# Performance work log

Measured on AMD Instinct MI355X. Metric: run time of the kernel, lower is better.

Reference implementation:

```python
import jax, jax.numpy as jnp
import numpy as np

L, B, D = 512, 16, 256
H = 4            # MAX_DIFF == num_heads
MAX_BONDS = 6
MAX_DIFF = 4
PROB_SHIFT = 0.3


def _attn_weights(x, Wqk, Wq, bq, Wk, bk, mask):
    """Per-head softmax(QK^T/sqrt(hd)) with key padding mask.
    x: [b,l,d]; Wqk: [d,2d] (the inc/dec_qk pre-projection);
    Wq/Wk: [d,d] (MHA in_proj, stored x@W layout); mask: [b,l] bool (True=masked).
    Returns [b,h,l,l]. The V path / out_proj of the torch MHA are discarded
    by the original module, so they are omitted here.
    """
    b, l, d = x.shape
    hd = d // H
    q = x @ Wqk[:, :d]
    k = x @ Wqk[:, d:]
    Q = (q @ Wq + bq).reshape(b, l, H, hd)
    K = (k @ Wk + bk).reshape(b, l, H, hd)
    scores = jnp.einsum('blhd,bmhd->bhlm', Q, K) / np.sqrt(hd)
    scores = jnp.where(mask[:, None, None, :], -jnp.inf, scores)
    return jax.nn.softmax(scores, axis=-1)


def setup_inputs() -> dict:
    key = jax.random.key(0)
    ks = jax.random.split(key, 16)
    s = 0.05
    p = lambda k, shape: jax.random.normal(k, shape, jnp.float32) * s
    # key_padding_mask: last 64 positions padded (True == masked)
    src_mask = jnp.broadcast_to(jnp.arange(L)[None, :] >= (L - 64), (B, L))
    return {
        'molecule_embedding': jax.random.normal(ks[0], (L, B, D), jnp.float32),
        'src_bond': jax.random.randint(ks[1], (B, L, MAX_BONDS), 0, L, jnp.int32),
        'src_mask': src_mask,
        'W_inc_qk': p(ks[2], (D, 2 * D)),
        'Wq_inc': p(ks[3], (D, D)), 'bq_inc': p(ks[4], (D,)),
        'Wk_inc': p(ks[5], (D, D)), 'bk_inc': p(ks[6], (D,)),
        'W_dec_qk': p(ks[7], (D, 2 * D)),
        'Wq_dec': p(ks[8], (D, D)), 'bq_dec': p(ks[9], (D,)),
        'Wk_dec': p(ks[10], (D, D)), 'bk_dec': p(ks[11], (D,)),
        'Wc': p(ks[12], (MAX_DIFF, MAX_DIFF)), 'bc': p(ks[13], (MAX_DIFF,)),
    }


def reference(molecule_embedding, src_bond, src_mask,
              W_inc_qk, Wq_inc, bq_inc, Wk_inc, bk_inc,
              W_dec_qk, Wq_dec, bq_dec, Wk_dec, bk_dec,
              Wc, bc):
    x = jnp.transpose(molecule_embedding, (1, 0, 2))  # [b,l,d]
    b, l, _ = x.shape

    inc = _attn_weights(x, W_inc_qk, Wq_inc, bq_inc, Wk_inc, bk_inc, src_mask)
    dec = _attn_weights(x, W_dec_qk, Wq_dec, bq_dec, Wk_dec, bk_dec, src_mask)

    pad = (~src_mask).astype(jnp.float32)              # 1 - mask
    pm2 = pad[:, :, None] * pad[:, None, :]            # [b,l,l]

    # cls_layer((inc-dec).permute(0,2,3,1)) * (MAX_DIFF*pad_mask)[...,None]
    diff = (jnp.einsum('bhlm,hc->blmc', inc - dec, Wc) + bc)
    diff = diff * (MAX_DIFF * pm2)[..., None]          # [b,l,l,4]

    # src_bond has last dim == MAX_BONDS -> one-hot neighbor counts
    src_w = jax.nn.one_hot(src_bond, l, dtype=jnp.float32).sum(axis=2) * pm2  # [b,l,l]
    eye = jnp.eye(l, dtype=jnp.float32)
    src_w = src_w * (1.0 - eye)[None]                  # zero diagonal

    # _shift_probs(src_weight.long(), prob_shift, MAX_DIFF)
    oh = jax.nn.one_hot(src_w.astype(jnp.int32), MAX_DIFF, dtype=jnp.float32)
    probs = oh * (1.0 - PROB_SHIFT) + (1.0 - oh) * (PROB_SHIFT / (MAX_DIFF - 1))
    probs = probs / probs.sum(axis=-1, keepdims=True)

    return jnp.log(probs + 1e-6) + diff                # [b,l,l,4]
```

## Files before the change

kernel.cpp:

```cpp
#include <hip/hip_runtime.h>
#include <stdint.h>

typedef unsigned short u16t;
typedef short s8v __attribute__((ext_vector_type(8)));
typedef float f4v __attribute__((ext_vector_type(4)));

#define MFMA16 __builtin_amdgcn_mfma_f32_16x16x32_bf16

#define QKN (16*4*512*64)

__device__ __forceinline__ u16t f2bf(float f) {
  unsigned u = __builtin_bit_cast(unsigned, f);
  u += 0x7fffu + ((u >> 16) & 1u);
  return (u16t)(u >> 16);
}

__global__ __launch_bounds__(256) void mask_norm(const int* __restrict__ raw,
                                                 int* __restrict__ dst) {
  __shared__ int mode;
  const int t = threadIdx.x;
  if (t == 0) mode = 0;
  __syncthreads();
  unsigned v0 = (unsigned)raw[t], v1 = (unsigned)raw[t + 256];
  if (v0 == 0x3F800000u || v1 == 0x3F800000u) mode = 2;
  __syncthreads();
  if (mode == 0 && (v0 > 1u || v1 > 1u)) mode = 1;
  __syncthreads();
  const int i = blockIdx.x * 256 + t;
  int m;
  if (mode == 2)      m = (((const float*)raw)[i] != 0.0f) ? 1 : 0;
  else if (mode == 1) m = ((const unsigned char*)raw)[i];
  else                m = raw[i];
  dst[i] = m;
}

__global__ __launch_bounds__(256) void weff_kernel(
    const float* __restrict__ Wiqk, const float* __restrict__ Wqi, const float* __restrict__ Wki,
    const float* __restrict__ Wdqk, const float* __restrict__ Wqd, const float* __restrict__ Wkd,
    u16t* __restrict__ weffT) {
  __shared__ float At[16][65];
  __shared__ float Bt[16][65];
  const int tid = threadIdx.x;
  const int n0 = blockIdx.x * 64;
  const int d0 = blockIdx.y * 64;
  const int p  = blockIdx.z;
  const float* A2  = (p == 0) ? Wqi : (p == 1) ? Wki : (p == 2) ? Wqd : Wkd;
  const float* Wqk = (p < 2) ? Wiqk : Wdqk;
  const int aoff = (p & 1) * 256;
  const int tx = tid & 15, ty = tid >> 4;

  float acc[4][4];
#pragma unroll
  for (int i = 0; i < 4; ++i)
#pragma unroll
    for (int j = 0; j < 4; ++j) acc[i][j] = 0.f;

  for (int k0 = 0; k0 < 256; k0 += 16) {
    __syncthreads();
    {
      int nn = tid & 63, kr = tid >> 6;
#pragma unroll
      for (int pass = 0; pass < 4; ++pass) {
        int kk = kr + pass * 4;
        At[kk][nn] = A2[(size_t)(k0 + kk) * 256 + n0 + nn];
      }
      int kk = tid & 15, dr = tid >> 4;
#pragma unroll
      for (int pass = 0; pass < 4; ++pass) {
        int dd = dr + pass * 16;
        Bt[kk][dd] = Wqk[(size_t)(d0 + dd) * 512 + aoff + k0 + kk];
      }
    }
    __syncthreads();
#pragma unroll
    for (int kk = 0; kk < 16; ++kk) {
      float a[4], b[4];
#pragma unroll
      for (int i = 0; i < 4; ++i) a[i] = At[kk][ty * 4 + i];
#pragma unroll
      for (int j = 0; j < 4; ++j) b[j] = Bt[kk][tx * 4 + j];
#pragma unroll
      for (int i = 0; i < 4; ++i)
#pragma unroll
        for (int j = 0; j < 4; ++j) acc[i][j] = fmaf(a[i], b[j], acc[i][j]);
    }
  }

#pragma unroll
  for (int i = 0; i < 4; ++i) {
    u16t h[4] = {f2bf(acc[i][0]), f2bf(acc[i][1]), f2bf(acc[i][2]), f2bf(acc[i][3])};
    *(uint2*)(&weffT[((size_t)(p * 256 + n0 + ty * 4 + i)) * 256 + d0 + tx * 4]) =
        *(const uint2*)h;
  }
}

__global__ __launch_bounds__(256) void proj_kernel(
    const float* __restrict__ emb, const u16t* __restrict__ weffT,
    const float* __restrict__ bq_inc, const float* __restrict__ bk_inc,
    const float* __restrict__ bq_dec, const float* __restrict__ bk_dec,
    u16t* __restrict__ qk) {
  __shared__ __align__(16) u16t As[128 * 40];
  __shared__ __align__(16) u16t Bs[128 * 40];
  const int t = threadIdx.x;
  const int n0 = blockIdx.x * 128;
  const int r0 = blockIdx.y * 128;
  const int bb = r0 >> 9;
  const int l0 = r0 & 511;
  const int lane = t & 63, wid = t >> 6;
  const int quad = lane >> 4, c15 = lane & 15;
  const int wm = wid >> 1, wn = wid & 1;

  f4v acc[4][4];
#pragma unroll
  for (int i = 0; i < 4; ++i)
#pragma unroll
    for (int j = 0; j < 4; ++j) acc[i][j] = f4v{0.f, 0.f, 0.f, 0.f};

  for (int k0 = 0; k0 < 256; k0 += 32) {
    __syncthreads();
#pragma unroll
    for (int i = 0; i < 2; ++i) {
      int c = t + i * 256;
      int m = c >> 2, off = (c & 3) * 8;
      const float* src = emb + (size_t)((l0 + m) * 16 + bb) * 256 + k0 + off;
      float4 x0 = *(const float4*)src;
      float4 x1 = *(const float4*)(src + 4);
      u16t h[8] = {f2bf(x0.x), f2bf(x0.y), f2bf(x0.z), f2bf(x0.w),
                   f2bf(x1.x), f2bf(x1.y), f2bf(x1.z), f2bf(x1.w)};
      *(uint4*)(&As[m * 40 + off]) = *(const uint4*)h;
      *(uint4*)(&Bs[m * 40 + off]) =
          *(const uint4*)(weffT + (size_t)(n0 + m) * 256 + k0 + off);
    }
    __syncthreads();
    s8v af[4], bf[4];
#pragma unroll
    for (int mi = 0; mi < 4; ++mi)
      af[mi] = *(const s8v*)(&As[(wm * 64 + mi * 16 + c15) * 40 + quad * 8]);
#pragma unroll
    for (int ni = 0; ni < 4; ++ni)
      bf[ni] = *(const s8v*)(&Bs[(wn * 64 + ni * 16 + c15) * 40 + quad * 8]);
#pragma unroll
    for (int mi = 0; mi < 4; ++mi)
#pragma unroll
      for (int ni = 0; ni < 4; ++ni)
        acc[mi][ni] = MFMA16(af[mi], bf[ni], acc[mi][ni], 0, 0, 0);
  }

  const float* biasP[4] = {bq_inc, bk_inc, bq_dec, bk_dec};
#pragma unroll
  for (int ni = 0; ni < 4; ++ni) {
    int n = n0 + wn * 64 + ni * 16 + c15;
    int p = n >> 8, h = (n >> 6) & 3, tt = n & 63, jj = n & 255;
    float bias = biasP[p][jj];
    u16t* dst = qk + (size_t)p * QKN;
#pragma unroll
    for (int mi = 0; mi < 4; ++mi) {
#pragma unroll
      for (int reg = 0; reg < 4; ++reg) {
        int l = l0 + wm * 64 + mi * 16 + quad * 4 + reg;
        dst[((size_t)(bb * 4 + h) * 512 + l) * 64 + tt] = f2bf(acc[mi][ni][reg] + bias);
      }
    }
  }
}

__global__ __launch_bounds__(256) void stats_kernel(
    const u16t* __restrict__ qk, const int* __restrict__ mask, float* __restrict__ invsum) {
  __shared__ __align__(16) u16t Qs[64 * 72];
  __shared__ __align__(16) u16t Ks[128 * 72];
  __shared__ int mrow[512];
  const int t = threadIdx.x;
  const int l0 = blockIdx.x * 64;
  const int cy = blockIdx.y;
  const int pp = cy >> 6, bb = (cy >> 2) & 15, h = cy & 3;
  const u16t* Q = qk + (size_t)(2 * pp) * QKN;
  const u16t* K = qk + (size_t)(2 * pp + 1) * QKN;
  mrow[t] = mask[bb * 512 + t];
  mrow[t + 256] = mask[bb * 512 + t + 256];
#pragma unroll
  for (int i = 0; i < 2; ++i) {
    int c = t + i * 256;
    int row = c >> 3, off = (c & 7) * 8;
    *(uint4*)(&Qs[row * 72 + off]) =
        *(const uint4*)(Q + ((size_t)(bb * 4 + h) * 512 + l0 + row) * 64 + off);
  }
  const int lane = t & 63, wid = t >> 6;
  const int quad = lane >> 4, c15 = lane & 15;
  float rs[4] = {0.f, 0.f, 0.f, 0.f};
  for (int m0 = 0; m0 < 512; m0 += 128) {
    __syncthreads();
#pragma unroll
    for (int i = 0; i < 4; ++i) {
      int c = t + i * 256;
      int row = c >> 3, off = (c & 7) * 8;
      *(uint4*)(&Ks[row * 72 + off]) =
          *(const uint4*)(K + ((size_t)(bb * 4 + h) * 512 + m0 + row) * 64 + off);
    }
    __syncthreads();
    s8v a0 = *(const s8v*)(&Qs[(wid * 16 + c15) * 72 + quad * 8]);
    s8v a1 = *(const s8v*)(&Qs[(wid * 16 + c15) * 72 + 32 + quad * 8]);
#pragma unroll
    for (int nt = 0; nt < 8; ++nt) {
      s8v b0 = *(const s8v*)(&Ks[(nt * 16 + c15) * 72 + quad * 8]);
      s8v b1 = *(const s8v*)(&Ks[(nt * 16 + c15) * 72 + 32 + quad * 8]);
      f4v sacc = f4v{0.f, 0.f, 0.f, 0.f};
      sacc = MFMA16(a0, b0, sacc, 0, 0, 0);
      sacc = MFMA16(a1, b1, sacc, 0, 0, 0);
      int m = m0 + nt * 16 + c15;
      if (!mrow[m]) {
#pragma unroll
        for (int reg = 0; reg < 4; ++reg) rs[reg] += __expf(sacc[reg] * 0.125f);
      }
    }
  }
#pragma unroll
  for (int reg = 0; reg < 4; ++reg) {
#pragma unroll
    for (int off = 1; off < 16; off <<= 1) rs[reg] += __shfl_xor(rs[reg], off);
  }
  if (c15 == 0) {
#pragma unroll
    for (int reg = 0; reg < 4; ++reg) {
      int l = l0 + wid * 16 + quad * 4 + reg;
      invsum[((size_t)(pp * 16 + bb) * 4 + h) * 512 + l] = 1.0f / rs[reg];
    }
  }
}

__global__ __launch_bounds__(256) void final_kernel(
    const u16t* __restrict__ qk, const int* __restrict__ mask, const float* __restrict__ invsum,
    const int* __restrict__ src_bond, const float* __restrict__ Wc, const float* __restrict__ bc,
    float* __restrict__ out) {
  __shared__ __align__(16) u16t Qs[8 * 16 * 72];
  __shared__ __align__(16) u16t Ks[128 * 72];
  __shared__ int bondsL[96];
  __shared__ int mlds[144];
  const int t = threadIdx.x;
  const int m0 = blockIdx.x * 128;
  const int l0 = blockIdx.y * 16;
  const int bb = blockIdx.z;

#pragma unroll
  for (int i = 0; i < 4; ++i) {
    int c = t + i * 256;
    int q = c >> 7, row = (c >> 3) & 15, off = (c & 7) * 8;
    const u16t* Qb = qk + (size_t)(2 * (q >> 2)) * QKN;
    *(uint4*)(&Qs[(q * 16 + row) * 72 + off]) =
        *(const uint4*)(Qb + ((size_t)(bb * 4 + (q & 3)) * 512 + l0 + row) * 64 + off);
  }
  if (t < 96) bondsL[t] = src_bond[(size_t)(bb * 512 + l0 + t / 6) * 6 + (t % 6)];
  if (t < 128) mlds[t] = mask[bb * 512 + m0 + t];
  else if (t < 144) mlds[t] = mask[bb * 512 + l0 + (t - 128)];

  const int lane = t & 63, wid = t >> 6;
  const int quad = lane >> 4, c15 = lane & 15;

  float Wf[16];
#pragma unroll
  for (int i = 0; i < 16; ++i) Wf[i] = Wc[i];

  float dacc[2][4][4];
#pragma unroll
  for (int a = 0; a < 2; ++a)
#pragma unroll
    for (int r = 0; r < 4; ++r)
#pragma unroll
      for (int c = 0; c < 4; ++c) dacc[a][r][c] = 0.f;

  for (int q = 0; q < 8; ++q) {
    const int pp = q >> 2, h = q & 3;
    __syncthreads();
#pragma unroll
    for (int i = 0; i < 4; ++i) {
      int c = t + i * 256;
      int row = c >> 3, off = (c & 7) * 8;
      const u16t* Kb = qk + (size_t)(2 * pp + 1) * QKN;
      *(uint4*)(&Ks[row * 72 + off]) =
          *(const uint4*)(Kb + ((size_t)(bb * 4 + h) * 512 + m0 + row) * 64 + off);
    }
    __syncthreads();
    s8v a0 = *(const s8v*)(&Qs[(q * 16 + c15) * 72 + quad * 8]);
    s8v a1 = *(const s8v*)(&Qs[(q * 16 + c15) * 72 + 32 + quad * 8]);
    float iv[4];
#pragma unroll
    for (int reg = 0; reg < 4; ++reg)
      iv[reg] = invsum[((size_t)(pp * 16 + bb) * 4 + h) * 512 + l0 + quad * 4 + reg];
#pragma unroll
    for (int nt = 0; nt < 2; ++nt) {
      int nrow = wid * 32 + nt * 16 + c15;
      s8v b0 = *(const s8v*)(&Ks[nrow * 72 + quad * 8]);
      s8v b1 = *(const s8v*)(&Ks[nrow * 72 + 32 + quad * 8]);
      f4v sacc = f4v{0.f, 0.f, 0.f, 0.f};
      sacc = MFMA16(a0, b0, sacc, 0, 0, 0);
      sacc = MFMA16(a1, b1, sacc, 0, 0, 0);
      if (!mlds[nrow]) {
#pragma unroll
        for (int reg = 0; reg < 4; ++reg) {
          float P = __expf(sacc[reg] * 0.125f) * iv[reg];
          if (pp) P = -P;
#pragma unroll
          for (int c = 0; c < 4; ++c)
            dacc[nt][reg][c] = fmaf(P, Wf[h * 4 + c], dacc[nt][reg][c]);
        }
      }
    }
  }

  float bcF[4];
#pragma unroll
  for (int c = 0; c < 4; ++c) bcF[c] = bc[c];
  const float lgH = logf(0.7f + 1e-6f);
  const float lgM = logf(0.1f + 1e-6f);
  const float lgU = logf(0.25f + 1e-6f);

#pragma unroll
  for (int nt = 0; nt < 2; ++nt) {
    int mloc = wid * 32 + nt * 16 + c15;
    int m = m0 + mloc;
    bool padm = (mlds[mloc] == 0);
#pragma unroll
    for (int reg = 0; reg < 4; ++reg) {
      int lloc = quad * 4 + reg;
      int l = l0 + lloc;
      bool padl = (mlds[128 + lloc] == 0);
      bool pm = padl && padm;
      int cnt = 0;
#pragma unroll
      for (int j = 0; j < 6; ++j) cnt += (bondsL[lloc * 6 + j] == m) ? 1 : 0;
      int cls = (pm && (m != l)) ? cnt : 0;
      float v[4];
#pragma unroll
      for (int c = 0; c < 4; ++c) {
        float lp = (cls >= 4) ? lgU : ((c == cls) ? lgH : lgM);
        float dv = pm ? 4.f * (dacc[nt][reg][c] + bcF[c]) : 0.f;
        v[c] = lp + dv;
      }
      float4 o = make_float4(v[0], v[1], v[2], v[3]);
      *(float4*)(&out[((size_t)(bb * 512 + l) * 512 + m) * 4]) = o;
    }
  }
}

extern "C" void kernel_launch(void* const* d_in, const int* in_sizes, int n_in,
                              void* d_out, int out_size, void* d_ws, size_t ws_size,
                              hipStream_t stream) {
  (void)in_sizes; (void)n_in; (void)out_size; (void)ws_size;
  const float* emb      = (const float*)d_in[0];
  const int*   src_bond = (const int*)d_in[1];
  const int*   mask_raw = (const int*)d_in[2];
  const float* W_inc_qk = (const float*)d_in[3];
  const float* Wq_inc   = (const float*)d_in[4];
  const float* bq_inc   = (const float*)d_in[5];
  const float* Wk_inc   = (const float*)d_in[6];
  const float* bk_inc   = (const float*)d_in[7];
  const float* W_dec_qk = (const float*)d_in[8];
  const float* Wq_dec   = (const float*)d_in[9];
  const float* bq_dec   = (const float*)d_in[10];
  const float* Wk_dec   = (const float*)d_in[11];
  const float* bk_dec   = (const float*)d_in[12];
  const float* Wc       = (const float*)d_in[13];
  const float* bc       = (const float*)d_in[14];
  float* out = (float*)d_out;

  char* ws = (char*)d_ws;
  int*   wsMask = (int*)ws;
  u16t*  weffT  = (u16t*)(ws + 32768);
  u16t*  qk     = (u16t*)(ws + 32768 + 524288);
  float* invsum = (float*)(ws + 32768 + 524288 + 16777216);

  hipLaunchKernelGGL(mask_norm,   dim3(32),         dim3(256), 0, stream, mask_raw, wsMask);
  hipLaunchKernelGGL(weff_kernel, dim3(4, 4, 4),    dim3(256), 0, stream,
                     W_inc_qk, Wq_inc, Wk_inc, W_dec_qk, Wq_dec, Wk_dec, weffT);
  hipLaunchKernelGGL(proj_kernel, dim3(8, 64),      dim3(256), 0, stream,
                     emb, weffT, bq_inc, bk_inc, bq_dec, bk_dec, qk);
  hipLaunchKernelGGL(stats_kernel, dim3(8, 128),    dim3(256), 0, stream, qk, wsMask, invsum);
  hipLaunchKernelGGL(final_kernel, dim3(4, 32, 16), dim3(256), 0, stream,
                     qk, wsMask, invsum, src_bond, Wc, bc, out);
}
```

Baseline: 179.3 us.

## Fuse softmax stats into final kernel and merge mask prep into weight prep

Merges the mask normalization kernel into the weight-preparation kernel as an extra grid slice, and removes the separate softmax-statistics pass. Each 512-thread block now covers a full 512-wide key row for 16 queries, computes row sums in-block through a shared-memory cross-wave reduction, and normalizes directly. This removes two launches, the invsum round trip and the duplicate QK^T recomputation. In exchange the grid shrinks to 512 blocks, K tiles are read straight from global memory into registers with no LDS staging, and each head step now needs a barrier.

```diff
diff --git a/kernel.cpp b/kernel.cpp
--- a/kernel.cpp
+++ b/kernel.cpp
@@ -6,7 +6,6 @@
 typedef float f4v __attribute__((ext_vector_type(4)));
 
 #define MFMA16 __builtin_amdgcn_mfma_f32_16x16x32_bf16
-
 #define QKN (16*4*512*64)
 
 __device__ __forceinline__ u16t f2bf(float f) {
@@ -15,32 +14,36 @@
   return (u16t)(u >> 16);
 }
 
-__global__ __launch_bounds__(256) void mask_norm(const int* __restrict__ raw,
-                                                 int* __restrict__ dst) {
-  __shared__ int mode;
-  const int t = threadIdx.x;
-  if (t == 0) mode = 0;
-  __syncthreads();
-  unsigned v0 = (unsigned)raw[t], v1 = (unsigned)raw[t + 256];
-  if (v0 == 0x3F800000u || v1 == 0x3F800000u) mode = 2;
-  __syncthreads();
-  if (mode == 0 && (v0 > 1u || v1 > 1u)) mode = 1;
-  __syncthreads();
-  const int i = blockIdx.x * 256 + t;
-  int m;
-  if (mode == 2)      m = (((const float*)raw)[i] != 0.0f) ? 1 : 0;
-  else if (mode == 1) m = ((const unsigned char*)raw)[i];
-  else                m = raw[i];
-  dst[i] = m;
-}
-
-__global__ __launch_bounds__(256) void weff_kernel(
+__global__ __launch_bounds__(256) void prep_kernel(
     const float* __restrict__ Wiqk, const float* __restrict__ Wqi, const float* __restrict__ Wki,
     const float* __restrict__ Wdqk, const float* __restrict__ Wqd, const float* __restrict__ Wkd,
-    u16t* __restrict__ weffT) {
+    u16t* __restrict__ weffT, const int* __restrict__ mraw, int* __restrict__ mdst) {
   __shared__ float At[16][65];
   __shared__ float Bt[16][65];
+  __shared__ int mode;
   const int tid = threadIdx.x;
+
+  if (blockIdx.z == 4) {
+    if (tid == 0) mode = 0;
+    __syncthreads();
+    unsigned v0 = (unsigned)mraw[tid], v1 = (unsigned)mraw[tid + 256];
+    if (v0 == 0x3F800000u || v1 == 0x3F800000u) mode = 2;
+    __syncthreads();
+    if (mode == 0 && (v0 > 1u || v1 > 1u)) mode = 1;
+    __syncthreads();
+    const int g = blockIdx.y * 4 + blockIdx.x;
+#pragma unroll
+    for (int i = 0; i < 2; ++i) {
+      int idx = g * 512 + i * 256 + tid;
+      int m;
+      if (mode == 2)      m = (((const float*)mraw)[idx] != 0.0f) ? 1 : 0;
+      else if (mode == 1) m = ((const unsigned char*)mraw)[idx];
+      else                m = mraw[idx];
+      mdst[idx] = m;
+    }
+    return;
+  }
+
   const int n0 = blockIdx.x * 64;
   const int d0 = blockIdx.y * 64;
   const int p  = blockIdx.z;
@@ -164,93 +167,29 @@
   }
 }
 
-__global__ __launch_bounds__(256) void stats_kernel(
-    const u16t* __restrict__ qk, const int* __restrict__ mask, float* __restrict__ invsum) {
-  __shared__ __align__(16) u16t Qs[64 * 72];
-  __shared__ __align__(16) u16t Ks[128 * 72];
-  __shared__ int mrow[512];
+__global__ __launch_bounds__(512) void fused_kernel(
+    const u16t* __restrict__ qk, const int* __restrict__ mask,
+    const int* __restrict__ src_bond, const float* __restrict__ Wc,
+    const float* __restrict__ bc, float* __restrict__ out) {
+  __shared__ __align__(16) u16t Qs[8 * 16 * 72];
+  __shared__ int bondsL[96];
+  __shared__ int mlds[512 + 16];
+  __shared__ float rpart[2][8][16];
   const int t = threadIdx.x;
-  const int l0 = blockIdx.x * 64;
-  const int cy = blockIdx.y;
-  const int pp = cy >> 6, bb = (cy >> 2) & 15, h = cy & 3;
-  const u16t* Q = qk + (size_t)(2 * pp) * QKN;
-  const u16t* K = qk + (size_t)(2 * pp + 1) * QKN;
-  mrow[t] = mask[bb * 512 + t];
-  mrow[t + 256] = mask[bb * 512 + t + 256];
+  const int l0 = blockIdx.x * 16;
+  const int bb = blockIdx.y;
+
 #pragma unroll
   for (int i = 0; i < 2; ++i) {
-    int c = t + i * 256;
-    int row = c >> 3, off = (c & 7) * 8;
-    *(uint4*)(&Qs[row * 72 + off]) =
-        *(const uint4*)(Q + ((size_t)(bb * 4 + h) * 512 + l0 + row) * 64 + off);
-  }
-  const int lane = t & 63, wid = t >> 6;
-  const int quad = lane >> 4, c15 = lane & 15;
-  float rs[4] = {0.f, 0.f, 0.f, 0.f};
-  for (int m0 = 0; m0 < 512; m0 += 128) {
-    __syncthreads();
-#pragma unroll
-    for (int i = 0; i < 4; ++i) {
-      int c = t + i * 256;
-      int row = c >> 3, off = (c & 7) * 8;
-      *(uint4*)(&Ks[row * 72 + off]) =
-          *(const uint4*)(K + ((size_t)(bb * 4 + h) * 512 + m0 + row) * 64 + off);
-    }
-    __syncthreads();
-    s8v a0 = *(const s8v*)(&Qs[(wid * 16 + c15) * 72 + quad * 8]);
-    s8v a1 = *(const s8v*)(&Qs[(wid * 16 + c15) * 72 + 32 + quad * 8]);
-#pragma unroll
-    for (int nt = 0; nt < 8; ++nt) {
-      s8v b0 = *(const s8v*)(&Ks[(nt * 16 + c15) * 72 + quad * 8]);
-      s8v b1 = *(const s8v*)(&Ks[(nt * 16 + c15) * 72 + 32 + quad * 8]);
-      f4v sacc = f4v{0.f, 0.f, 0.f, 0.f};
-      sacc = MFMA16(a0, b0, sacc, 0, 0, 0);
-      sacc = MFMA16(a1, b1, sacc, 0, 0, 0);
-      int m = m0 + nt * 16 + c15;
-      if (!mrow[m]) {
-#pragma unroll
-        for (int reg = 0; reg < 4; ++reg) rs[reg] += __expf(sacc[reg] * 0.125f);
-      }
-    }
-  }
-#pragma unroll
-  for (int reg = 0; reg < 4; ++reg) {
-#pragma unroll
-    for (int off = 1; off < 16; off <<= 1) rs[reg] += __shfl_xor(rs[reg], off);
-  }
-  if (c15 == 0) {
-#pragma unroll
-    for (int reg = 0; reg < 4; ++reg) {
-      int l = l0 + wid * 16 + quad * 4 + reg;
-      invsum[((size_t)(pp * 16 + bb) * 4 + h) * 512 + l] = 1.0f / rs[reg];
-    }
-  }
-}
-
-__global__ __launch_bounds__(256) void final_kernel(
-    const u16t* __restrict__ qk, const int* __restrict__ mask, const float* __restrict__ invsum,
-    const int* __restrict__ src_bond, const float* __restrict__ Wc, const float* __restrict__ bc,
-    float* __restrict__ out) {
-  __shared__ __align__(16) u16t Qs[8 * 16 * 72];
-  __shared__ __align__(16) u16t Ks[128 * 72];
-  __shared__ int bondsL[96];
-  __shared__ int mlds[144];
-  const int t = threadIdx.x;
-  const int m0 = blockIdx.x * 128;
-  const int l0 = blockIdx.y * 16;
-  const int bb = blockIdx.z;
-
-#pragma unroll
-  for (int i = 0; i < 4; ++i) {
-    int c = t + i * 256;
+    int c = t + i * 512;
     int q = c >> 7, row = (c >> 3) & 15, off = (c & 7) * 8;
     const u16t* Qb = qk + (size_t)(2 * (q >> 2)) * QKN;
     *(uint4*)(&Qs[(q * 16 + row) * 72 + off]) =
         *(const uint4*)(Qb + ((size_t)(bb * 4 + (q & 3)) * 512 + l0 + row) * 64 + off);
   }
+  mlds[t] = mask[bb * 512 + t];
+  if (t < 16) mlds[512 + t] = mask[bb * 512 + l0 + t];
   if (t < 96) bondsL[t] = src_bond[(size_t)(bb * 512 + l0 + t / 6) * 6 + (t % 6)];
-  if (t < 128) mlds[t] = mask[bb * 512 + m0 + t];
-  else if (t < 144) mlds[t] = mask[bb * 512 + l0 + (t - 128)];
 
   const int lane = t & 63, wid = t >> 6;
   const int quad = lane >> 4, c15 = lane & 15;
@@ -259,49 +198,77 @@
 #pragma unroll
   for (int i = 0; i < 16; ++i) Wf[i] = Wc[i];
 
-  float dacc[2][4][4];
-#pragma unroll
-  for (int a = 0; a < 2; ++a)
+  float dacc[4][4][4];
+#pragma unroll
+  for (int nt = 0; nt < 4; ++nt)
 #pragma unroll
     for (int r = 0; r < 4; ++r)
 #pragma unroll
-      for (int c = 0; c < 4; ++c) dacc[a][r][c] = 0.f;
-
+      for (int c = 0; c < 4; ++c) dacc[nt][r][c] = 0.f;
+
+  __syncthreads();
+
+#pragma unroll 1
   for (int q = 0; q < 8; ++q) {
     const int pp = q >> 2, h = q & 3;
-    __syncthreads();
-#pragma unroll
-    for (int i = 0; i < 4; ++i) {
-      int c = t + i * 256;
-      int row = c >> 3, off = (c & 7) * 8;
-      const u16t* Kb = qk + (size_t)(2 * pp + 1) * QKN;
-      *(uint4*)(&Ks[row * 72 + off]) =
-          *(const uint4*)(Kb + ((size_t)(bb * 4 + h) * 512 + m0 + row) * 64 + off);
-    }
-    __syncthreads();
+    const u16t* Kb = qk + (size_t)(2 * pp + 1) * QKN + (size_t)(bb * 4 + h) * 512 * 64;
     s8v a0 = *(const s8v*)(&Qs[(q * 16 + c15) * 72 + quad * 8]);
     s8v a1 = *(const s8v*)(&Qs[(q * 16 + c15) * 72 + 32 + quad * 8]);
-    float iv[4];
-#pragma unroll
-    for (int reg = 0; reg < 4; ++reg)
-      iv[reg] = invsum[((size_t)(pp * 16 + bb) * 4 + h) * 512 + l0 + quad * 4 + reg];
-#pragma unroll
-    for (int nt = 0; nt < 2; ++nt) {
-      int nrow = wid * 32 + nt * 16 + c15;
-      s8v b0 = *(const s8v*)(&Ks[nrow * 72 + quad * 8]);
-      s8v b1 = *(const s8v*)(&Ks[nrow * 72 + 32 + quad * 8]);
+
+    s8v kb0[4], kb1[4];
+#pragma unroll
+    for (int nt = 0; nt < 4; ++nt) {
+      int m = wid * 64 + nt * 16 + c15;
+      kb0[nt] = *(const s8v*)(Kb + (size_t)m * 64 + quad * 8);
+      kb1[nt] = *(const s8v*)(Kb + (size_t)m * 64 + 32 + quad * 8);
+    }
+
+    float E[4][4];
+    float rsum[4] = {0.f, 0.f, 0.f, 0.f};
+#pragma unroll
+    for (int nt = 0; nt < 4; ++nt) {
       f4v sacc = f4v{0.f, 0.f, 0.f, 0.f};
-      sacc = MFMA16(a0, b0, sacc, 0, 0, 0);
-      sacc = MFMA16(a1, b1, sacc, 0, 0, 0);
-      if (!mlds[nrow]) {
-#pragma unroll
-        for (int reg = 0; reg < 4; ++reg) {
-          float P = __expf(sacc[reg] * 0.125f) * iv[reg];
-          if (pp) P = -P;
-#pragma unroll
-          for (int c = 0; c < 4; ++c)
-            dacc[nt][reg][c] = fmaf(P, Wf[h * 4 + c], dacc[nt][reg][c]);
-        }
+      sacc = MFMA16(a0, kb0[nt], sacc, 0, 0, 0);
+      sacc = MFMA16(a1, kb1[nt], sacc, 0, 0, 0);
+      int m = wid * 64 + nt * 16 + c15;
+      bool msk = (mlds[m] != 0);
+#pragma unroll
+      for (int reg = 0; reg < 4; ++reg) {
+        float e = msk ? 0.f : __expf(sacc[reg] * 0.125f);
+        E[nt][reg] = e;
+        rsum[reg] += e;
+      }
+    }
+
+#pragma unroll
+    for (int reg = 0; reg < 4; ++reg) {
+#pragma unroll
+      for (int off = 1; off < 16; off <<= 1) rsum[reg] += __shfl_xor(rsum[reg], off);
+    }
+    if (c15 == 0) {
+#pragma unroll
+      for (int reg = 0; reg < 4; ++reg) rpart[q & 1][wid][quad * 4 + reg] = rsum[reg];
+    }
+    __syncthreads();
+
+    float inv[4];
+    const float sgn = pp ? -1.f : 1.f;
+#pragma unroll
+    for (int reg = 0; reg < 4; ++reg) {
+      float tot = 0.f;
+#pragma unroll
+      for (int w = 0; w < 8; ++w) tot += rpart[q & 1][w][quad * 4 + reg];
+      inv[reg] = sgn / tot;
+    }
+
+#pragma unroll
+    for (int nt = 0; nt < 4; ++nt) {
+#pragma unroll
+      for (int reg = 0; reg < 4; ++reg) {
+        float P = E[nt][reg] * inv[reg];
+#pragma unroll
+        for (int c = 0; c < 4; ++c)
+          dacc[nt][reg][c] = fmaf(P, Wf[h * 4 + c], dacc[nt][reg][c]);
       }
     }
   }
@@ -314,15 +281,14 @@
   const float lgU = logf(0.25f + 1e-6f);
 
 #pragma unroll
-  for (int nt = 0; nt < 2; ++nt) {
-    int mloc = wid * 32 + nt * 16 + c15;
-    int m = m0 + mloc;
-    bool padm = (mlds[mloc] == 0);
+  for (int nt = 0; nt < 4; ++nt) {
+    int m = wid * 64 + nt * 16 + c15;
+    bool padm = (mlds[m] == 0);
 #pragma unroll
     for (int reg = 0; reg < 4; ++reg) {
       int lloc = quad * 4 + reg;
       int l = l0 + lloc;
-      bool padl = (mlds[128 + lloc] == 0);
+      bool padl = (mlds[512 + lloc] == 0);
       bool pm = padl && padm;
       int cnt = 0;
 #pragma unroll
@@ -366,14 +332,12 @@
   int*   wsMask = (int*)ws;
   u16t*  weffT  = (u16t*)(ws + 32768);
   u16t*  qk     = (u16t*)(ws + 32768 + 524288);
-  float* invsum = (float*)(ws + 32768 + 524288 + 16777216);
-
-  hipLaunchKernelGGL(mask_norm,   dim3(32),         dim3(256), 0, stream, mask_raw, wsMask);
-  hipLaunchKernelGGL(weff_kernel, dim3(4, 4, 4),    dim3(256), 0, stream,
-                     W_inc_qk, Wq_inc, Wk_inc, W_dec_qk, Wq_dec, Wk_dec, weffT);
-  hipLaunchKernelGGL(proj_kernel, dim3(8, 64),      dim3(256), 0, stream,
+
+  hipLaunchKernelGGL(prep_kernel, dim3(4, 4, 5), dim3(256), 0, stream,
+                     W_inc_qk, Wq_inc, Wk_inc, W_dec_qk, Wq_dec, Wk_dec, weffT,
+                     mask_raw, wsMask);
+  hipLaunchKernelGGL(proj_kernel, dim3(8, 64), dim3(256), 0, stream,
                      emb, weffT, bq_inc, bk_inc, bq_dec, bk_dec, qk);
-  hipLaunchKernelGGL(stats_kernel, dim3(8, 128),    dim3(256), 0, stream, qk, wsMask, invsum);
-  hipLaunchKernelGGL(final_kernel, dim3(4, 32, 16), dim3(256), 0, stream,
-                     qk, wsMask, invsum, src_bond, Wc, bc, out);
-}
+  hipLaunchKernelGGL(fused_kernel, dim3(32, 16), dim3(512), 0, stream,
+                     qk, wsMask, src_bond, Wc, bc, out);
+}
```

New measurement: 195.2 us. 8.9% more time.
